# Kernel optimization log

Measured on AMD Instinct MI355X. Metric: run time of the kernel, lower is better.

## Reference

```python
import jax, jax.numpy as jnp
import numpy as np

N_NODES = 50000
N_EDGES = 640000
D_IN = 128
D_H1 = 128
D_H2 = 128
N_CLASSES = 64


def setup_inputs() -> dict:
    key = jax.random.key(0)
    ks = jax.random.split(key, 8)
    x = jax.random.normal(ks[0], (N_NODES, D_IN), dtype=jnp.float32)
    edge_index = jax.random.randint(ks[1], (2, N_EDGES), 0, N_NODES, dtype=jnp.int64)
    s1 = 1.0 / np.sqrt(D_IN)
    s2 = 1.0 / np.sqrt(D_H1)
    s3 = 1.0 / np.sqrt(D_H2)
    W1 = jax.random.uniform(ks[2], (D_IN, D_H1), jnp.float32, -s1, s1)
    b1 = jnp.zeros((D_H1,), jnp.float32)
    W2 = jax.random.uniform(ks[3], (D_H1, D_H2), jnp.float32, -s2, s2)
    b2 = jnp.zeros((D_H2,), jnp.float32)
    Wl = jax.random.uniform(ks[4], (D_H2, N_CLASSES), jnp.float32, -s3, s3)
    bl = jax.random.uniform(ks[5], (N_CLASSES,), jnp.float32, -s3, s3)
    return {"x": x, "edge_index": edge_index, "W1": W1, "b1": b1,
            "W2": W2, "b2": b2, "Wl": Wl, "bl": bl}


def _gcn_norm(edge_index, num_nodes):
    # PyG GCNConv: add self-loops, symmetric normalization D^-1/2 (A+I) D^-1/2
    loop = jnp.arange(num_nodes, dtype=edge_index.dtype)
    src = jnp.concatenate([edge_index[0], loop])
    dst = jnp.concatenate([edge_index[1], loop])
    deg = jax.ops.segment_sum(jnp.ones_like(dst, dtype=jnp.float32), dst,
                              num_segments=num_nodes)
    dinv = jnp.where(deg > 0, jax.lax.rsqrt(deg), 0.0)
    norm = dinv[src] * dinv[dst]  # [E+N]
    return src, dst, norm


def _gcn_conv(h, src, dst, norm, W, b, num_nodes):
    h = h @ W                       # transform first (smaller gather when D_out small)
    msg = h[src] * norm[:, None]    # gather + per-edge scale  [E+N, D_out]
    agg = jax.ops.segment_sum(msg, dst, num_segments=num_nodes)  # scatter-add
    return agg + b


def reference(x, edge_index, W1, b1, W2, b2, Wl, bl):
    n = x.shape[0]
    src, dst, norm = _gcn_norm(edge_index, n)
    h = jax.nn.relu(_gcn_conv(x, src, dst, norm, W1, b1, n))
    # dropout is identity in eval mode
    h = jax.nn.relu(_gcn_conv(h, src, dst, norm, W2, b2, n))
    return h @ Wl + bl
```

## Files before the change

kernel.cpp:

```cpp
#include <hip/hip_runtime.h>


typedef __attribute__((ext_vector_type(8))) __bf16 bf16x8;
typedef __attribute__((ext_vector_type(8))) short short8;
typedef __attribute__((ext_vector_type(4))) float f32x4;

__device__ inline float bf_lo(unsigned u) { return __uint_as_float(u << 16); }
__device__ inline float bf_hi(unsigned u) { return __uint_as_float(u & 0xffff0000u); }
__device__ inline unsigned short f2bf(float v) {
  return __builtin_bit_cast(unsigned short, (__bf16)v);
}

__global__ void k_count(const int* __restrict__ dst, int E, int* __restrict__ cnt) {
  int i = blockIdx.x * blockDim.x + threadIdx.x;
  if (i < E) atomicAdd(&cnt[dst[i]], 1);
}

__global__ void k_scan1_prepW(const int* __restrict__ cnt, int n, int* __restrict__ partial,
                              int nb,
                              const float* __restrict__ W1, const float* __restrict__ W2,
                              const float* __restrict__ Wl,
                              unsigned short* __restrict__ b1h, unsigned short* __restrict__ b1l,
                              unsigned short* __restrict__ b2h, unsigned short* __restrict__ b2l,
                              unsigned short* __restrict__ blh, unsigned short* __restrict__ bll) {
  if ((int)blockIdx.x < nb) {
    __shared__ int s[256];
    int i = blockIdx.x * 256 + threadIdx.x;
    s[threadIdx.x] = (i < n) ? cnt[i] : 0;
    __syncthreads();
    for (int off = 128; off > 0; off >>= 1) {
      if (threadIdx.x < off) s[threadIdx.x] += s[threadIdx.x + off];
      __syncthreads();
    }
    if (threadIdx.x == 0) partial[blockIdx.x] = s[0];
  } else {
    int idx = ((int)blockIdx.x - nb) * 256 + threadIdx.x;
    const float* W;
    unsigned short *bh, *bl_;
    int N, local;
    if (idx < 16384)      { W = W1; bh = b1h; bl_ = b1l; N = 128; local = idx; }
    else if (idx < 32768) { W = W2; bh = b2h; bl_ = b2l; N = 128; local = idx - 16384; }
    else if (idx < 40960) { W = Wl; bh = blh; bl_ = bll; N = 64;  local = idx - 32768; }
    else return;
    int nn = local >> 7, k = local & 127;
    float v = W[(size_t)k * N + nn];
    __bf16 h = (__bf16)v;
    bh[local] = __builtin_bit_cast(unsigned short, h);
    bl_[local] = f2bf(v - (float)h);
  }
}

__global__ void k_scan3(const int* __restrict__ cnt, const int* __restrict__ partial,
                        int nb, int n, int* __restrict__ row_off, int* __restrict__ cursor,
                        float* __restrict__ dinv) {
  __shared__ int s[256];
  __shared__ int base_s;
  int t = threadIdx.x;
  s[t] = (t < nb && t < (int)blockIdx.x) ? partial[t] : 0;
  __syncthreads();
  for (int off = 128; off > 0; off >>= 1) {
    if (t < off) s[t] += s[t + off];
    __syncthreads();
  }
  if (t == 0) base_s = s[0];
  __syncthreads();
  int base = base_s;
  __syncthreads();

  int i = blockIdx.x * 256 + t;
  int v = (i < n) ? cnt[i] : 0;
  s[t] = v;
  __syncthreads();
  for (int off = 1; off < 256; off <<= 1) {
    int u = (t >= off) ? s[t - off] : 0;
    __syncthreads();
    s[t] += u;
    __syncthreads();
  }
  int incl = s[t];
  int excl = incl - v;
  if (i < n) {
    row_off[i] = base + excl;
    cursor[i] = base + excl;
    dinv[i] = rsqrtf((float)(v + 1));
    if (i == n - 1) row_off[n] = base + incl;
  }
}

__global__ void k_place(const int* __restrict__ src, const int* __restrict__ dst, int E,
                        int* __restrict__ cursor, const float* __restrict__ dinv,
                        unsigned long long* __restrict__ edges) {
  int e = blockIdx.x * blockDim.x + threadIdx.x;
  if (e < E) {
    int s = src[e], d = dst[e];
    int pos = atomicAdd(&cursor[d], 1);
    unsigned long long packed =
        (unsigned long long)(unsigned)s |
        ((unsigned long long)__float_as_uint(dinv[s] * dinv[d]) << 32);
    __builtin_nontemporal_store(packed, &edges[pos]);
  }
}

template <int NT, bool A32, bool BIAS, bool OUT_BF16>
__global__ __launch_bounds__(256) void gemm3(
    const void* __restrict__ Ahi_, const unsigned short* __restrict__ Alo,
    const unsigned short* __restrict__ Bhi, const unsigned short* __restrict__ Blo,
    const float* __restrict__ bias, void* __restrict__ Cout, int M) {
  constexpr int K = 128;
  constexpr int NCOL = NT * 16;
  __shared__ alignas(16) unsigned short lbh[NCOL * K];
  __shared__ alignas(16) unsigned short lbl[NCOL * K];
  int t = threadIdx.x;
  int lane = t & 63, wave = t >> 6;
  int lm = lane & 15, lk = lane >> 4;
  int m_base = blockIdx.x * 128 + wave * 32;
  const short8 zero8 = {0, 0, 0, 0, 0, 0, 0, 0};

  bf16x8 ah[2][4], al[2][4];
  if (A32) {
    const float* Af = (const float*)Ahi_;
    float4 ra[2][4][2];
#pragma unroll
    for (int mt = 0; mt < 2; ++mt) {
      int row = m_base + mt * 16 + lm;
#pragma unroll
      for (int ks = 0; ks < 4; ++ks) {
        if (row < M) {
          ra[mt][ks][0] = *(const float4*)&Af[(size_t)row * K + ks * 32 + lk * 8];
          ra[mt][ks][1] = *(const float4*)&Af[(size_t)row * K + ks * 32 + lk * 8 + 4];
        } else {
          ra[mt][ks][0] = make_float4(0.f, 0.f, 0.f, 0.f);
          ra[mt][ks][1] = make_float4(0.f, 0.f, 0.f, 0.f);
        }
      }
    }
#pragma unroll
    for (int mt = 0; mt < 2; ++mt)
#pragma unroll
      for (int ks = 0; ks < 4; ++ks) {
        float av[8] = {ra[mt][ks][0].x, ra[mt][ks][0].y, ra[mt][ks][0].z, ra[mt][ks][0].w,
                       ra[mt][ks][1].x, ra[mt][ks][1].y, ra[mt][ks][1].z, ra[mt][ks][1].w};
#pragma unroll
        for (int j = 0; j < 8; ++j) {
          __bf16 h = (__bf16)av[j];
          ah[mt][ks][j] = h;
          al[mt][ks][j] = (__bf16)(av[j] - (float)h);
        }
      }
  } else {
    const unsigned short* Ahi = (const unsigned short*)Ahi_;
#pragma unroll
    for (int mt = 0; mt < 2; ++mt) {
      int row = m_base + mt * 16 + lm;
#pragma unroll
      for (int ks = 0; ks < 4; ++ks) {
        if (row < M) {
          ah[mt][ks] = *(const bf16x8*)&Ahi[(size_t)row * K + ks * 32 + lk * 8];
          al[mt][ks] = *(const bf16x8*)&Alo[(size_t)row * K + ks * 32 + lk * 8];
        } else {
          ah[mt][ks] = __builtin_bit_cast(bf16x8, zero8);
          al[mt][ks] = __builtin_bit_cast(bf16x8, zero8);
        }
      }
    }
  }

  for (int c = t; c < NCOL * 16; c += 256) {
    int r = c >> 4, q = c & 15;
    int sq = q ^ (r & 15);
    *(short8*)&lbh[r * K + sq * 8] = *(const short8*)&Bhi[r * K + q * 8];
    *(short8*)&lbl[r * K + sq * 8] = *(const short8*)&Blo[r * K + q * 8];
  }
  __syncthreads();

  f32x4 acc[2][NT] = {};
#pragma unroll
  for (int ks = 0; ks < 4; ++ks) {
    int chunk = ks * 4 + lk;
    bf16x8 bh[NT], bl[NT];
#pragma unroll
    for (int nt = 0; nt < NT; ++nt) {
      int r = nt * 16 + lm;
      int sq = chunk ^ lm;
      bh[nt] = *(const bf16x8*)&lbh[r * K + sq * 8];
      bl[nt] = *(const bf16x8*)&lbl[r * K + sq * 8];
    }
#pragma unroll
    for (int mt = 0; mt < 2; ++mt)
#pragma unroll
      for (int nt = 0; nt < NT; ++nt) {
        acc[mt][nt] = __builtin_amdgcn_mfma_f32_16x16x32_bf16(ah[mt][ks], bh[nt], acc[mt][nt], 0, 0, 0);
        acc[mt][nt] = __builtin_amdgcn_mfma_f32_16x16x32_bf16(ah[mt][ks], bl[nt], acc[mt][nt], 0, 0, 0);
        acc[mt][nt] = __builtin_amdgcn_mfma_f32_16x16x32_bf16(al[mt][ks], bh[nt], acc[mt][nt], 0, 0, 0);
      }
  }

#pragma unroll
  for (int mt = 0; mt < 2; ++mt) {
#pragma unroll
    for (int r = 0; r < 4; ++r) {
      int row = m_base + mt * 16 + lk * 4 + r;
      if (row < M) {
#pragma unroll
        for (int nt = 0; nt < NT; ++nt) {
          int col = nt * 16 + lm;
          float v = acc[mt][nt][r];
          if (BIAS) v += bias[col];
          if (OUT_BF16)
            ((unsigned short*)Cout)[(size_t)row * NCOL + col] = f2bf(v);
          else
            __builtin_nontemporal_store(v, &((float*)Cout)[(size_t)row * NCOL + col]);
        }
      }
    }
  }
}

__global__ __launch_bounds__(256) void k_agg(const unsigned short* __restrict__ t,
                      const int* __restrict__ row_off,
                      const int2* __restrict__ edges,
                      const float* __restrict__ dinv, const float* __restrict__ bias,
                      unsigned short* __restrict__ ghi, unsigned short* __restrict__ glo,
                      int n) {
  int wave = threadIdx.x >> 6;
  int lane = threadIdx.x & 63;
  int g = lane >> 4;
  int fl = lane & 15;
  int node = blockIdx.x * 4 + wave;
  if (node >= n) return;
  int e0 = row_off[node], e1 = row_off[node + 1];
  int last = e1 - 1;

  float acc[8] = {};
  for (int base = e0; base < e1; base += 8) {
    int i0 = base + g, i1 = base + 4 + g;
    int c0 = i0 < e1 ? i0 : last;
    int c1 = i1 < e1 ? i1 : last;
    int2 p0 = edges[c0];
    int2 p1 = edges[c1];
    uint4 u0 = *(const uint4*)&t[(size_t)p0.x * 128 + fl * 8];
    uint4 u1 = *(const uint4*)&t[(size_t)p1.x * 128 + fl * 8];
    float w0 = i0 < e1 ? __int_as_float(p0.y) : 0.f;
    float w1 = i1 < e1 ? __int_as_float(p1.y) : 0.f;
    acc[0] += w0 * bf_lo(u0.x); acc[1] += w0 * bf_hi(u0.x);
    acc[2] += w0 * bf_lo(u0.y); acc[3] += w0 * bf_hi(u0.y);
    acc[4] += w0 * bf_lo(u0.z); acc[5] += w0 * bf_hi(u0.z);
    acc[6] += w0 * bf_lo(u0.w); acc[7] += w0 * bf_hi(u0.w);
    acc[0] += w1 * bf_lo(u1.x); acc[1] += w1 * bf_hi(u1.x);
    acc[2] += w1 * bf_lo(u1.y); acc[3] += w1 * bf_hi(u1.y);
    acc[4] += w1 * bf_lo(u1.z); acc[5] += w1 * bf_hi(u1.z);
    acc[6] += w1 * bf_lo(u1.w); acc[7] += w1 * bf_hi(u1.w);
  }
#pragma unroll
  for (int j = 0; j < 8; ++j) {
    acc[j] += __shfl_xor(acc[j], 16);
    acc[j] += __shfl_xor(acc[j], 32);
  }
  if (g == 0) {
    float di = dinv[node];
    float self = di * di;
    uint4 sv = *(const uint4*)&t[(size_t)node * 128 + fl * 8];
    acc[0] += self * bf_lo(sv.x); acc[1] += self * bf_hi(sv.x);
    acc[2] += self * bf_lo(sv.y); acc[3] += self * bf_hi(sv.y);
    acc[4] += self * bf_lo(sv.z); acc[5] += self * bf_hi(sv.z);
    acc[6] += self * bf_lo(sv.w); acc[7] += self * bf_hi(sv.w);
    float4 bb0 = *(const float4*)&bias[fl * 8];
    float4 bb1 = *(const float4*)&bias[fl * 8 + 4];
    float bb[8] = {bb0.x, bb0.y, bb0.z, bb0.w, bb1.x, bb1.y, bb1.z, bb1.w};
    short8 ho, lo_;
#pragma unroll
    for (int j = 0; j < 8; ++j) {
      float s = fmaxf(acc[j] + bb[j], 0.f);
      __bf16 h = (__bf16)s;
      ho[j] = __builtin_bit_cast(short, h);
      lo_[j] = (short)f2bf(s - (float)h);
    }
    *(short8*)&ghi[(size_t)node * 128 + fl * 8] = ho;
    *(short8*)&glo[(size_t)node * 128 + fl * 8] = lo_;
  }
}

extern "C" void kernel_launch(void* const* d_in, const int* in_sizes, int n_in,
                              void* d_out, int out_size, void* d_ws, size_t ws_size,
                              hipStream_t stream) {
  const float* x  = (const float*)d_in[0];
  const int*   ei = (const int*)d_in[1];
  const float* W1 = (const float*)d_in[2];
  const float* b1 = (const float*)d_in[3];
  const float* W2 = (const float*)d_in[4];
  const float* b2 = (const float*)d_in[5];
  const float* Wl = (const float*)d_in[6];
  const float* bl = (const float*)d_in[7];
  float* out = (float*)d_out;

  const int D = 128;
  int N = in_sizes[0] / D;
  int E = in_sizes[1] / 2;
  const int* src = ei;
  const int* dst = ei + E;

  uintptr_t ws = (uintptr_t)d_ws;
  auto take = [&](size_t bytes) {
    uintptr_t p = ws;
    ws += (bytes + 15) & ~(size_t)15;
    return p;
  };
  unsigned short* t_bf = (unsigned short*)take((size_t)N * D * 2);
  unsigned short* xh   = (unsigned short*)take((size_t)N * D * 2);
  unsigned short* xl   = (unsigned short*)take((size_t)N * D * 2);
  unsigned long long* edges = (unsigned long long*)take((size_t)E * 8);
  int*   cnt     = (int*)take((size_t)N * sizeof(int));
  int*   row_off = (int*)take(((size_t)N + 1) * sizeof(int));
  int*   cursor  = (int*)take((size_t)N * sizeof(int));
  float* dinv    = (float*)take((size_t)N * sizeof(float));
  int*   partial = (int*)take(256 * sizeof(int));
  unsigned short* b1h = (unsigned short*)take(128 * 128 * 2);
  unsigned short* b1l = (unsigned short*)take(128 * 128 * 2);
  unsigned short* b2h = (unsigned short*)take(128 * 128 * 2);
  unsigned short* b2l = (unsigned short*)take(128 * 128 * 2);
  unsigned short* blh = (unsigned short*)take(128 * 64 * 2);
  unsigned short* bll = (unsigned short*)take(128 * 64 * 2);

  int nb_n = (N + 255) / 256;
  int nb_e = (E + 255) / 256;

  hipMemsetAsync(cnt, 0, (size_t)N * sizeof(int), stream);
  k_count<<<nb_e, 256, 0, stream>>>(dst, E, cnt);
  k_scan1_prepW<<<nb_n + 160, 256, 0, stream>>>(cnt, N, partial, nb_n,
                                                W1, W2, Wl, b1h, b1l, b2h, b2l, blh, bll);
  k_scan3<<<nb_n, 256, 0, stream>>>(cnt, partial, nb_n, N, row_off, cursor, dinv);
  k_place<<<nb_e, 256, 0, stream>>>(src, dst, E, cursor, dinv, edges);

  int gemm_blocks = (N + 127) / 128;
  int agg_blocks = (N + 3) / 4;

  gemm3<8, true, false, true><<<gemm_blocks, 256, 0, stream>>>(x, nullptr, b1h, b1l, nullptr, t_bf, N);
  k_agg<<<agg_blocks, 256, 0, stream>>>(t_bf, row_off, (const int2*)edges, dinv, b1, xh, xl, N);
  gemm3<8, false, false, true><<<gemm_blocks, 256, 0, stream>>>(xh, xl, b2h, b2l, nullptr, t_bf, N);
  k_agg<<<agg_blocks, 256, 0, stream>>>(t_bf, row_off, (const int2*)edges, dinv, b2, xh, xl, N);
  gemm3<4, false, true, false><<<gemm_blocks, 256, 0, stream>>>(xh, xl, blh, bll, bl, out, N);
}
```

Measured before the change: 246.5 us.

## Fuse graph preprocessing into one persistent kernel and factor normalization into GEMM epilogue

```diff
diff --git a/kernel.cpp b/kernel.cpp
--- a/kernel.cpp
+++ b/kernel.cpp
@@ -11,101 +11,116 @@
   return __builtin_bit_cast(unsigned short, (__bf16)v);
 }
 
-__global__ void k_count(const int* __restrict__ dst, int E, int* __restrict__ cnt) {
-  int i = blockIdx.x * blockDim.x + threadIdx.x;
-  if (i < E) atomicAdd(&cnt[dst[i]], 1);
-}
-
-__global__ void k_scan1_prepW(const int* __restrict__ cnt, int n, int* __restrict__ partial,
-                              int nb,
-                              const float* __restrict__ W1, const float* __restrict__ W2,
-                              const float* __restrict__ Wl,
-                              unsigned short* __restrict__ b1h, unsigned short* __restrict__ b1l,
-                              unsigned short* __restrict__ b2h, unsigned short* __restrict__ b2l,
-                              unsigned short* __restrict__ blh, unsigned short* __restrict__ bll) {
-  if ((int)blockIdx.x < nb) {
-    __shared__ int s[256];
-    int i = blockIdx.x * 256 + threadIdx.x;
-    s[threadIdx.x] = (i < n) ? cnt[i] : 0;
-    __syncthreads();
-    for (int off = 128; off > 0; off >>= 1) {
-      if (threadIdx.x < off) s[threadIdx.x] += s[threadIdx.x + off];
-      __syncthreads();
-    }
-    if (threadIdx.x == 0) partial[blockIdx.x] = s[0];
-  } else {
-    int idx = ((int)blockIdx.x - nb) * 256 + threadIdx.x;
-    const float* W;
-    unsigned short *bh, *bl_;
-    int N, local;
-    if (idx < 16384)      { W = W1; bh = b1h; bl_ = b1l; N = 128; local = idx; }
-    else if (idx < 32768) { W = W2; bh = b2h; bl_ = b2l; N = 128; local = idx - 16384; }
-    else if (idx < 40960) { W = Wl; bh = blh; bl_ = bll; N = 64;  local = idx - 32768; }
-    else return;
-    int nn = local >> 7, k = local & 127;
-    float v = W[(size_t)k * N + nn];
-    __bf16 h = (__bf16)v;
-    bh[local] = __builtin_bit_cast(unsigned short, h);
-    bl_[local] = f2bf(v - (float)h);
-  }
-}
-
-__global__ void k_scan3(const int* __restrict__ cnt, const int* __restrict__ partial,
-                        int nb, int n, int* __restrict__ row_off, int* __restrict__ cursor,
-                        float* __restrict__ dinv) {
+__device__ inline void gbar(int* bar, int phase, int nblk) {
+  __syncthreads();
+  if (threadIdx.x == 0) {
+    __threadfence();
+    atomicAdd(&bar[phase], 1);
+    while (__hip_atomic_load(&bar[phase], __ATOMIC_RELAXED,
+                             __HIP_MEMORY_SCOPE_AGENT) < nblk) {
+      __builtin_amdgcn_s_sleep(8);
+    }
+    __threadfence();
+  }
+  __syncthreads();
+}
+
+#define MEGA_BLOCKS 1024
+#define CNT_BLOCKS 960
+
+__global__ __launch_bounds__(256, 8) void k_mega(
+    const int* __restrict__ src, const int* __restrict__ dst, int E, int N, int nb,
+    int* __restrict__ cnt, int* __restrict__ bar, int* __restrict__ partial,
+    int* __restrict__ row_off, int* __restrict__ cursor, float* __restrict__ dinv,
+    int* __restrict__ edges,
+    const float* __restrict__ W1, const float* __restrict__ W2,
+    const float* __restrict__ Wl,
+    unsigned short* __restrict__ b1h, unsigned short* __restrict__ b1l,
+    unsigned short* __restrict__ b2h, unsigned short* __restrict__ b2l,
+    unsigned short* __restrict__ blh, unsigned short* __restrict__ bll) {
+  int t = threadIdx.x;
+  int b = blockIdx.x;
   __shared__ int s[256];
   __shared__ int base_s;
-  int t = threadIdx.x;
-  s[t] = (t < nb && t < (int)blockIdx.x) ? partial[t] : 0;
-  __syncthreads();
-  for (int off = 128; off > 0; off >>= 1) {
-    if (t < off) s[t] += s[t + off];
-    __syncthreads();
-  }
-  if (t == 0) base_s = s[0];
-  __syncthreads();
-  int base = base_s;
-  __syncthreads();
-
-  int i = blockIdx.x * 256 + t;
-  int v = (i < n) ? cnt[i] : 0;
-  s[t] = v;
-  __syncthreads();
-  for (int off = 1; off < 256; off <<= 1) {
-    int u = (t >= off) ? s[t - off] : 0;
-    __syncthreads();
-    s[t] += u;
-    __syncthreads();
-  }
-  int incl = s[t];
-  int excl = incl - v;
-  if (i < n) {
-    row_off[i] = base + excl;
-    cursor[i] = base + excl;
-    dinv[i] = rsqrtf((float)(v + 1));
-    if (i == n - 1) row_off[n] = base + incl;
-  }
-}
-
-__global__ void k_place(const int* __restrict__ src, const int* __restrict__ dst, int E,
-                        int* __restrict__ cursor, const float* __restrict__ dinv,
-                        unsigned long long* __restrict__ edges) {
-  int e = blockIdx.x * blockDim.x + threadIdx.x;
-  if (e < E) {
-    int s = src[e], d = dst[e];
+
+  if (b < CNT_BLOCKS) {
+    for (int i = b * 256 + t; i < E; i += CNT_BLOCKS * 256)
+      atomicAdd(&cnt[dst[i]], 1);
+  } else {
+    for (int idx = (b - CNT_BLOCKS) * 256 + t; idx < 40960;
+         idx += (MEGA_BLOCKS - CNT_BLOCKS) * 256) {
+      const float* W;
+      unsigned short *bh, *bl_;
+      int NN, local;
+      if (idx < 16384)      { W = W1; bh = b1h; bl_ = b1l; NN = 128; local = idx; }
+      else if (idx < 32768) { W = W2; bh = b2h; bl_ = b2l; NN = 128; local = idx - 16384; }
+      else                  { W = Wl; bh = blh; bl_ = bll; NN = 64;  local = idx - 32768; }
+      int nn = local >> 7, k = local & 127;
+      float v = W[(size_t)k * NN + nn];
+      __bf16 h = (__bf16)v;
+      bh[local] = __builtin_bit_cast(unsigned short, h);
+      bl_[local] = f2bf(v - (float)h);
+    }
+  }
+  gbar(bar, 0, MEGA_BLOCKS);
+
+  if (b < nb) {
+    int i = b * 256 + t;
+    s[t] = (i < N) ? cnt[i] : 0;
+    __syncthreads();
+    for (int off = 128; off > 0; off >>= 1) {
+      if (t < off) s[t] += s[t + off];
+      __syncthreads();
+    }
+    if (t == 0) partial[b] = s[0];
+  }
+  gbar(bar, 1, MEGA_BLOCKS);
+
+  if (b < nb) {
+    s[t] = (t < nb && t < b) ? partial[t] : 0;
+    __syncthreads();
+    for (int off = 128; off > 0; off >>= 1) {
+      if (t < off) s[t] += s[t + off];
+      __syncthreads();
+    }
+    if (t == 0) base_s = s[0];
+    __syncthreads();
+    int base = base_s;
+    __syncthreads();
+    int i = b * 256 + t;
+    int v = (i < N) ? cnt[i] : 0;
+    s[t] = v;
+    __syncthreads();
+    for (int off = 1; off < 256; off <<= 1) {
+      int u = (t >= off) ? s[t - off] : 0;
+      __syncthreads();
+      s[t] += u;
+      __syncthreads();
+    }
+    int incl = s[t];
+    int excl = incl - v;
+    if (i < N) {
+      row_off[i] = base + excl;
+      cursor[i] = base + excl;
+      dinv[i] = rsqrtf((float)(v + 1));
+      if (i == N - 1) row_off[N] = base + incl;
+    }
+  }
+  gbar(bar, 2, MEGA_BLOCKS);
+
+  for (int e = b * 256 + t; e < E; e += MEGA_BLOCKS * 256) {
+    int ss = src[e], d = dst[e];
     int pos = atomicAdd(&cursor[d], 1);
-    unsigned long long packed =
-        (unsigned long long)(unsigned)s |
-        ((unsigned long long)__float_as_uint(dinv[s] * dinv[d]) << 32);
-    __builtin_nontemporal_store(packed, &edges[pos]);
-  }
-}
-
-template <int NT, bool A32, bool BIAS, bool OUT_BF16>
+    __builtin_nontemporal_store(ss, &edges[pos]);
+  }
+}
+
+template <int NT, bool A32, bool BIAS, bool OUT_BF16, bool SCALE>
 __global__ __launch_bounds__(256) void gemm3(
     const void* __restrict__ Ahi_, const unsigned short* __restrict__ Alo,
     const unsigned short* __restrict__ Bhi, const unsigned short* __restrict__ Blo,
-    const float* __restrict__ bias, void* __restrict__ Cout, int M) {
+    const float* __restrict__ bias, const float* __restrict__ dinv,
+    void* __restrict__ Cout, int M) {
   constexpr int K = 128;
   constexpr int NCOL = NT * 16;
   __shared__ alignas(16) unsigned short lbh[NCOL * K];
@@ -116,6 +131,10 @@
   int m_base = blockIdx.x * 128 + wave * 32;
   const short8 zero8 = {0, 0, 0, 0, 0, 0, 0, 0};
 
+  if (SCALE && blockIdx.x == 0 && t < 64) {
+    *(unsigned*)&((unsigned short*)Cout)[(size_t)M * NCOL + t * 2] = 0u;
+  }
+
   bf16x8 ah[2][4], al[2][4];
   if (A32) {
     const float* Af = (const float*)Ahi_;
@@ -201,10 +220,12 @@
     for (int r = 0; r < 4; ++r) {
       int row = m_base + mt * 16 + lk * 4 + r;
       if (row < M) {
+        float dr = SCALE ? dinv[row] : 1.f;
 #pragma unroll
         for (int nt = 0; nt < NT; ++nt) {
           int col = nt * 16 + lm;
           float v = acc[mt][nt][r];
+          if (SCALE) v *= dr;
           if (BIAS) v += bias[col];
           if (OUT_BF16)
             ((unsigned short*)Cout)[(size_t)row * NCOL + col] = f2bf(v);
@@ -218,7 +239,7 @@
 
 __global__ __launch_bounds__(256) void k_agg(const unsigned short* __restrict__ t,
                       const int* __restrict__ row_off,
-                      const int2* __restrict__ edges,
+                      const int* __restrict__ edges,
                       const float* __restrict__ dinv, const float* __restrict__ bias,
                       unsigned short* __restrict__ ghi, unsigned short* __restrict__ glo,
                       int n) {
@@ -234,22 +255,20 @@
   float acc[8] = {};
   for (int base = e0; base < e1; base += 8) {
     int i0 = base + g, i1 = base + 4 + g;
-    int c0 = i0 < e1 ? i0 : last;
-    int c1 = i1 < e1 ? i1 : last;
-    int2 p0 = edges[c0];
-    int2 p1 = edges[c1];
-    uint4 u0 = *(const uint4*)&t[(size_t)p0.x * 128 + fl * 8];
-    uint4 u1 = *(const uint4*)&t[(size_t)p1.x * 128 + fl * 8];
-    float w0 = i0 < e1 ? __int_as_float(p0.y) : 0.f;
-    float w1 = i1 < e1 ? __int_as_float(p1.y) : 0.f;
-    acc[0] += w0 * bf_lo(u0.x); acc[1] += w0 * bf_hi(u0.x);
-    acc[2] += w0 * bf_lo(u0.y); acc[3] += w0 * bf_hi(u0.y);
-    acc[4] += w0 * bf_lo(u0.z); acc[5] += w0 * bf_hi(u0.z);
-    acc[6] += w0 * bf_lo(u0.w); acc[7] += w0 * bf_hi(u0.w);
-    acc[0] += w1 * bf_lo(u1.x); acc[1] += w1 * bf_hi(u1.x);
-    acc[2] += w1 * bf_lo(u1.y); acc[3] += w1 * bf_hi(u1.y);
-    acc[4] += w1 * bf_lo(u1.z); acc[5] += w1 * bf_hi(u1.z);
-    acc[6] += w1 * bf_lo(u1.w); acc[7] += w1 * bf_hi(u1.w);
+    int s0 = edges[i0 < e1 ? i0 : last];
+    int s1 = edges[i1 < e1 ? i1 : last];
+    s0 = i0 < e1 ? s0 : n;
+    s1 = i1 < e1 ? s1 : n;
+    uint4 u0 = *(const uint4*)&t[(size_t)s0 * 128 + fl * 8];
+    uint4 u1 = *(const uint4*)&t[(size_t)s1 * 128 + fl * 8];
+    acc[0] += bf_lo(u0.x) + bf_lo(u1.x);
+    acc[1] += bf_hi(u0.x) + bf_hi(u1.x);
+    acc[2] += bf_lo(u0.y) + bf_lo(u1.y);
+    acc[3] += bf_hi(u0.y) + bf_hi(u1.y);
+    acc[4] += bf_lo(u0.z) + bf_lo(u1.z);
+    acc[5] += bf_hi(u0.z) + bf_hi(u1.z);
+    acc[6] += bf_lo(u0.w) + bf_lo(u1.w);
+    acc[7] += bf_hi(u0.w) + bf_hi(u1.w);
   }
 #pragma unroll
   for (int j = 0; j < 8; ++j) {
@@ -258,19 +277,18 @@
   }
   if (g == 0) {
     float di = dinv[node];
-    float self = di * di;
     uint4 sv = *(const uint4*)&t[(size_t)node * 128 + fl * 8];
-    acc[0] += self * bf_lo(sv.x); acc[1] += self * bf_hi(sv.x);
-    acc[2] += self * bf_lo(sv.y); acc[3] += self * bf_hi(sv.y);
-    acc[4] += self * bf_lo(sv.z); acc[5] += self * bf_hi(sv.z);
-    acc[6] += self * bf_lo(sv.w); acc[7] += self * bf_hi(sv.w);
+    acc[0] += bf_lo(sv.x); acc[1] += bf_hi(sv.x);
+    acc[2] += bf_lo(sv.y); acc[3] += bf_hi(sv.y);
+    acc[4] += bf_lo(sv.z); acc[5] += bf_hi(sv.z);
+    acc[6] += bf_lo(sv.w); acc[7] += bf_hi(sv.w);
     float4 bb0 = *(const float4*)&bias[fl * 8];
     float4 bb1 = *(const float4*)&bias[fl * 8 + 4];
     float bb[8] = {bb0.x, bb0.y, bb0.z, bb0.w, bb1.x, bb1.y, bb1.z, bb1.w};
     short8 ho, lo_;
 #pragma unroll
     for (int j = 0; j < 8; ++j) {
-      float s = fmaxf(acc[j] + bb[j], 0.f);
+      float s = fmaxf(acc[j] * di + bb[j], 0.f);
       __bf16 h = (__bf16)s;
       ho[j] = __builtin_bit_cast(short, h);
       lo_[j] = (short)f2bf(s - (float)h);
@@ -305,11 +323,12 @@
     ws += (bytes + 15) & ~(size_t)15;
     return p;
   };
-  unsigned short* t_bf = (unsigned short*)take((size_t)N * D * 2);
+  unsigned short* t_bf = (unsigned short*)take(((size_t)N + 1) * D * 2);
   unsigned short* xh   = (unsigned short*)take((size_t)N * D * 2);
   unsigned short* xl   = (unsigned short*)take((size_t)N * D * 2);
-  unsigned long long* edges = (unsigned long long*)take((size_t)E * 8);
-  int*   cnt     = (int*)take((size_t)N * sizeof(int));
+  int*   edges   = (int*)take((size_t)E * 4);
+  int*   cnt     = (int*)take((size_t)N * sizeof(int) + 16);
+  int*   bar     = cnt + N;
   int*   row_off = (int*)take(((size_t)N + 1) * sizeof(int));
   int*   cursor  = (int*)take((size_t)N * sizeof(int));
   float* dinv    = (float*)take((size_t)N * sizeof(float));
@@ -322,21 +341,21 @@
   unsigned short* bll = (unsigned short*)take(128 * 64 * 2);
 
   int nb_n = (N + 255) / 256;
-  int nb_e = (E + 255) / 256;
-
-  hipMemsetAsync(cnt, 0, (size_t)N * sizeof(int), stream);
-  k_count<<<nb_e, 256, 0, stream>>>(dst, E, cnt);
-  k_scan1_prepW<<<nb_n + 160, 256, 0, stream>>>(cnt, N, partial, nb_n,
-                                                W1, W2, Wl, b1h, b1l, b2h, b2l, blh, bll);
-  k_scan3<<<nb_n, 256, 0, stream>>>(cnt, partial, nb_n, N, row_off, cursor, dinv);
-  k_place<<<nb_e, 256, 0, stream>>>(src, dst, E, cursor, dinv, edges);
+
+  hipMemsetAsync(cnt, 0, (size_t)N * sizeof(int) + 16, stream);
+  k_mega<<<MEGA_BLOCKS, 256, 0, stream>>>(src, dst, E, N, nb_n,
+                                          cnt, bar, partial, row_off, cursor, dinv, edges,
+                                          W1, W2, Wl, b1h, b1l, b2h, b2l, blh, bll);
 
   int gemm_blocks = (N + 127) / 128;
   int agg_blocks = (N + 3) / 4;
 
-  gemm3<8, true, false, true><<<gemm_blocks, 256, 0, stream>>>(x, nullptr, b1h, b1l, nullptr, t_bf, N);
-  k_agg<<<agg_blocks, 256, 0, stream>>>(t_bf, row_off, (const int2*)edges, dinv, b1, xh, xl, N);
-  gemm3<8, false, false, true><<<gemm_blocks, 256, 0, stream>>>(xh, xl, b2h, b2l, nullptr, t_bf, N);
-  k_agg<<<agg_blocks, 256, 0, stream>>>(t_bf, row_off, (const int2*)edges, dinv, b2, xh, xl, N);
-  gemm3<4, false, true, false><<<gemm_blocks, 256, 0, stream>>>(xh, xl, blh, bll, bl, out, N);
-}
+  gemm3<8, true, false, true, true><<<gemm_blocks, 256, 0, stream>>>(
+      x, nullptr, b1h, b1l, nullptr, dinv, t_bf, N);
+  k_agg<<<agg_blocks, 256, 0, stream>>>(t_bf, row_off, edges, dinv, b1, xh, xl, N);
+  gemm3<8, false, false, true, true><<<gemm_blocks, 256, 0, stream>>>(
+      xh, xl, b2h, b2l, nullptr, dinv, t_bf, N);
+  k_agg<<<agg_blocks, 256, 0, stream>>>(t_bf, row_off, edges, dinv, b2, xh, xl, N);
+  gemm3<4, false, true, false, false><<<gemm_blocks, 256, 0, stream>>>(
+      xh, xl, blh, bll, bl, nullptr, out, N);
+}
```

Measured after the change: 535.5 us. 117% more time.

## Fold symmetric normalization into GEMM row scale and aggregation epilogue

Applied to the files above, without the earlier changes.

```diff
diff --git a/kernel.cpp b/kernel.cpp
--- a/kernel.cpp
+++ b/kernel.cpp
@@ -88,24 +88,21 @@
 }
 
 __global__ void k_place(const int* __restrict__ src, const int* __restrict__ dst, int E,
-                        int* __restrict__ cursor, const float* __restrict__ dinv,
-                        unsigned long long* __restrict__ edges) {
+                        int* __restrict__ cursor, int* __restrict__ edges) {
   int e = blockIdx.x * blockDim.x + threadIdx.x;
   if (e < E) {
     int s = src[e], d = dst[e];
     int pos = atomicAdd(&cursor[d], 1);
-    unsigned long long packed =
-        (unsigned long long)(unsigned)s |
-        ((unsigned long long)__float_as_uint(dinv[s] * dinv[d]) << 32);
-    __builtin_nontemporal_store(packed, &edges[pos]);
-  }
-}
-
-template <int NT, bool A32, bool BIAS, bool OUT_BF16>
+    __builtin_nontemporal_store(s, &edges[pos]);
+  }
+}
+
+template <int NT, bool A32, bool BIAS, bool OUT_BF16, bool SCALE>
 __global__ __launch_bounds__(256) void gemm3(
     const void* __restrict__ Ahi_, const unsigned short* __restrict__ Alo,
     const unsigned short* __restrict__ Bhi, const unsigned short* __restrict__ Blo,
-    const float* __restrict__ bias, void* __restrict__ Cout, int M) {
+    const float* __restrict__ bias, const float* __restrict__ dinv,
+    void* __restrict__ Cout, int M) {
   constexpr int K = 128;
   constexpr int NCOL = NT * 16;
   __shared__ alignas(16) unsigned short lbh[NCOL * K];
@@ -116,6 +113,10 @@
   int m_base = blockIdx.x * 128 + wave * 32;
   const short8 zero8 = {0, 0, 0, 0, 0, 0, 0, 0};
 
+  if (SCALE && blockIdx.x == 0 && t < 64) {
+    *(unsigned*)&((unsigned short*)Cout)[(size_t)M * NCOL + t * 2] = 0u;
+  }
+
   bf16x8 ah[2][4], al[2][4];
   if (A32) {
     const float* Af = (const float*)Ahi_;
@@ -201,10 +202,12 @@
     for (int r = 0; r < 4; ++r) {
       int row = m_base + mt * 16 + lk * 4 + r;
       if (row < M) {
+        float dr = SCALE ? dinv[row] : 1.f;
 #pragma unroll
         for (int nt = 0; nt < NT; ++nt) {
           int col = nt * 16 + lm;
           float v = acc[mt][nt][r];
+          if (SCALE) v *= dr;
           if (BIAS) v += bias[col];
           if (OUT_BF16)
             ((unsigned short*)Cout)[(size_t)row * NCOL + col] = f2bf(v);
@@ -218,7 +221,7 @@
 
 __global__ __launch_bounds__(256) void k_agg(const unsigned short* __restrict__ t,
                       const int* __restrict__ row_off,
-                      const int2* __restrict__ edges,
+                      const int* __restrict__ edges,
                       const float* __restrict__ dinv, const float* __restrict__ bias,
                       unsigned short* __restrict__ ghi, unsigned short* __restrict__ glo,
                       int n) {
@@ -234,22 +237,20 @@
   float acc[8] = {};
   for (int base = e0; base < e1; base += 8) {
     int i0 = base + g, i1 = base + 4 + g;
-    int c0 = i0 < e1 ? i0 : last;
-    int c1 = i1 < e1 ? i1 : last;
-    int2 p0 = edges[c0];
-    int2 p1 = edges[c1];
-    uint4 u0 = *(const uint4*)&t[(size_t)p0.x * 128 + fl * 8];
-    uint4 u1 = *(const uint4*)&t[(size_t)p1.x * 128 + fl * 8];
-    float w0 = i0 < e1 ? __int_as_float(p0.y) : 0.f;
-    float w1 = i1 < e1 ? __int_as_float(p1.y) : 0.f;
-    acc[0] += w0 * bf_lo(u0.x); acc[1] += w0 * bf_hi(u0.x);
-    acc[2] += w0 * bf_lo(u0.y); acc[3] += w0 * bf_hi(u0.y);
-    acc[4] += w0 * bf_lo(u0.z); acc[5] += w0 * bf_hi(u0.z);
-    acc[6] += w0 * bf_lo(u0.w); acc[7] += w0 * bf_hi(u0.w);
-    acc[0] += w1 * bf_lo(u1.x); acc[1] += w1 * bf_hi(u1.x);
-    acc[2] += w1 * bf_lo(u1.y); acc[3] += w1 * bf_hi(u1.y);
-    acc[4] += w1 * bf_lo(u1.z); acc[5] += w1 * bf_hi(u1.z);
-    acc[6] += w1 * bf_lo(u1.w); acc[7] += w1 * bf_hi(u1.w);
+    int s0 = edges[i0 < e1 ? i0 : last];
+    int s1 = edges[i1 < e1 ? i1 : last];
+    s0 = i0 < e1 ? s0 : n;
+    s1 = i1 < e1 ? s1 : n;
+    uint4 u0 = *(const uint4*)&t[(size_t)s0 * 128 + fl * 8];
+    uint4 u1 = *(const uint4*)&t[(size_t)s1 * 128 + fl * 8];
+    acc[0] += bf_lo(u0.x) + bf_lo(u1.x);
+    acc[1] += bf_hi(u0.x) + bf_hi(u1.x);
+    acc[2] += bf_lo(u0.y) + bf_lo(u1.y);
+    acc[3] += bf_hi(u0.y) + bf_hi(u1.y);
+    acc[4] += bf_lo(u0.z) + bf_lo(u1.z);
+    acc[5] += bf_hi(u0.z) + bf_hi(u1.z);
+    acc[6] += bf_lo(u0.w) + bf_lo(u1.w);
+    acc[7] += bf_hi(u0.w) + bf_hi(u1.w);
   }
 #pragma unroll
   for (int j = 0; j < 8; ++j) {
@@ -258,19 +259,18 @@
   }
   if (g == 0) {
     float di = dinv[node];
-    float self = di * di;
     uint4 sv = *(const uint4*)&t[(size_t)node * 128 + fl * 8];
-    acc[0] += self * bf_lo(sv.x); acc[1] += self * bf_hi(sv.x);
-    acc[2] += self * bf_lo(sv.y); acc[3] += self * bf_hi(sv.y);
-    acc[4] += self * bf_lo(sv.z); acc[5] += self * bf_hi(sv.z);
-    acc[6] += self * bf_lo(sv.w); acc[7] += self * bf_hi(sv.w);
+    acc[0] += bf_lo(sv.x); acc[1] += bf_hi(sv.x);
+    acc[2] += bf_lo(sv.y); acc[3] += bf_hi(sv.y);
+    acc[4] += bf_lo(sv.z); acc[5] += bf_hi(sv.z);
+    acc[6] += bf_lo(sv.w); acc[7] += bf_hi(sv.w);
     float4 bb0 = *(const float4*)&bias[fl * 8];
     float4 bb1 = *(const float4*)&bias[fl * 8 + 4];
     float bb[8] = {bb0.x, bb0.y, bb0.z, bb0.w, bb1.x, bb1.y, bb1.z, bb1.w};
     short8 ho, lo_;
 #pragma unroll
     for (int j = 0; j < 8; ++j) {
-      float s = fmaxf(acc[j] + bb[j], 0.f);
+      float s = fmaxf(acc[j] * di + bb[j], 0.f);
       __bf16 h = (__bf16)s;
       ho[j] = __builtin_bit_cast(short, h);
       lo_[j] = (short)f2bf(s - (float)h);
@@ -305,10 +305,10 @@
     ws += (bytes + 15) & ~(size_t)15;
     return p;
   };
-  unsigned short* t_bf = (unsigned short*)take((size_t)N * D * 2);
+  unsigned short* t_bf = (unsigned short*)take(((size_t)N + 1) * D * 2);
   unsigned short* xh   = (unsigned short*)take((size_t)N * D * 2);
   unsigned short* xl   = (unsigned short*)take((size_t)N * D * 2);
-  unsigned long long* edges = (unsigned long long*)take((size_t)E * 8);
+  int*   edges   = (int*)take((size_t)E * 4);
   int*   cnt     = (int*)take((size_t)N * sizeof(int));
   int*   row_off = (int*)take(((size_t)N + 1) * sizeof(int));
   int*   cursor  = (int*)take((size_t)N * sizeof(int));
@@ -329,14 +329,17 @@
   k_scan1_prepW<<<nb_n + 160, 256, 0, stream>>>(cnt, N, partial, nb_n,
                                                 W1, W2, Wl, b1h, b1l, b2h, b2l, blh, bll);
   k_scan3<<<nb_n, 256, 0, stream>>>(cnt, partial, nb_n, N, row_off, cursor, dinv);
-  k_place<<<nb_e, 256, 0, stream>>>(src, dst, E, cursor, dinv, edges);
+  k_place<<<nb_e, 256, 0, stream>>>(src, dst, E, cursor, edges);
 
   int gemm_blocks = (N + 127) / 128;
   int agg_blocks = (N + 3) / 4;
 
-  gemm3<8, true, false, true><<<gemm_blocks, 256, 0, stream>>>(x, nullptr, b1h, b1l, nullptr, t_bf, N);
-  k_agg<<<agg_blocks, 256, 0, stream>>>(t_bf, row_off, (const int2*)edges, dinv, b1, xh, xl, N);
-  gemm3<8, false, false, true><<<gemm_blocks, 256, 0, stream>>>(xh, xl, b2h, b2l, nullptr, t_bf, N);
-  k_agg<<<agg_blocks, 256, 0, stream>>>(t_bf, row_off, (const int2*)edges, dinv, b2, xh, xl, N);
-  gemm3<4, false, true, false><<<gemm_blocks, 256, 0, stream>>>(xh, xl, blh, bll, bl, out, N);
-}
+  gemm3<8, true, false, true, true><<<gemm_blocks, 256, 0, stream>>>(
+      x, nullptr, b1h, b1l, nullptr, dinv, t_bf, N);
+  k_agg<<<agg_blocks, 256, 0, stream>>>(t_bf, row_off, edges, dinv, b1, xh, xl, N);
+  gemm3<8, false, false, true, true><<<gemm_blocks, 256, 0, stream>>>(
+      xh, xl, b2h, b2l, nullptr, dinv, t_bf, N);
+  k_agg<<<agg_blocks, 256, 0, stream>>>(t_bf, row_off, edges, dinv, b2, xh, xl, N);
+  gemm3<4, false, true, false, false><<<gemm_blocks, 256, 0, stream>>>(
+      xh, xl, blh, bll, bl, nullptr, out, N);
+}
```

Result: slower. 254.3 us (+3.2%).
